# Kernel tuning notes

Measured on AMD Instinct MI355X. Metric: run time of the kernel, lower is better.

## Reference

```python
import jax, jax.numpy as jnp
import numpy as np

N_NODES = 500_000
N_EDGES = 8_000_000
BN_EPS = 1e-5


def _graph_embed(src, dst, n, W_init, b_init, Wg, bg, Wt1, g1, b1, Wt2, g2, b2, Wd, bd):
    # init_graph: input is all-ones [n, 12] -> Linear(12->4); every row identical
    x_row = W_init.sum(0) + b_init                      # [4]
    h_row = jax.nn.sigmoid(x_row @ Wg + bg)             # node gating -> [7]
    h = jnp.broadcast_to(h_row, (n, h_row.shape[0]))    # [n, 7]

    # symmetric normalization, DGL TAGConv style
    deg = jnp.zeros((n,), jnp.float32).at[dst].add(1.0)
    norm = jnp.clip(deg, 1.0) ** -0.5                   # [n]

    def prop(x):  # x: [n, d] -> normalized adjacency propagation
        x = x * norm[:, None]
        agg = jnp.zeros_like(x).at[dst].add(x[src])
        return agg * norm[:, None]

    def tagconv(x, W):  # K=2: concat [h, Ah, A^2h] then linear (no bias)
        f1 = prop(x)
        f2 = prop(f1)
        return jnp.concatenate([x, f1, f2], axis=1) @ W

    def bn_relu(x, gamma, beta):  # BatchNorm1d training-mode (batch stats)
        m = x.mean(0)
        v = x.var(0)
        return jax.nn.relu((x - m) / jnp.sqrt(v + BN_EPS) * gamma + beta)

    h = bn_relu(tagconv(h, Wt1), g1, b1)
    h = bn_relu(tagconv(h, Wt2), g2, b2)
    h = h @ Wd + bd                                     # [n, 11]
    return h.mean(0)                                    # [11] graph embedding


def setup_inputs() -> dict:
    key = jax.random.key(0)
    ks = jax.random.split(key, 32)
    n, e = N_NODES, N_EDGES
    d = {
        "src1": jax.random.randint(ks[0], (e,), 0, n, dtype=jnp.int32),
        "dst1": jax.random.randint(ks[1], (e,), 0, n, dtype=jnp.int32),
        "src2": jax.random.randint(ks[2], (e,), 0, n, dtype=jnp.int32),
        "dst2": jax.random.randint(ks[3], (e,), 0, n, dtype=jnp.int32),
        "n_nodes": n,
    }
    def w(k, shape):
        return jax.random.normal(k, shape, jnp.float32) * 0.1
    # GraphEmbed params (node_emb=4, size_graph_emb=11, layers=(7,7), TAGConv K=2)
    d["W_init"] = w(ks[4], (12, 4)); d["b_init"] = w(ks[5], (4,))
    d["Wg"] = w(ks[6], (4, 7));      d["bg"] = w(ks[7], (7,))
    d["Wt1"] = w(ks[8], (21, 7))
    d["bn1_g"] = jnp.ones((7,), jnp.float32); d["bn1_b"] = jnp.zeros((7,), jnp.float32)
    d["Wt2"] = w(ks[9], (21, 7))
    d["bn2_g"] = jnp.ones((7,), jnp.float32); d["bn2_b"] = jnp.zeros((7,), jnp.float32)
    d["Wd"] = w(ks[10], (7, 11));    d["bd"] = w(ks[11], (11,))
    # GraphSimilarity params (embedding_space=11, layers=(7,7,7), 12 properties)
    d["Ws0"] = w(ks[12], (22, 7));   d["bs0"] = w(ks[13], (7,))
    d["Ws1"] = w(ks[14], (7, 7));    d["bs1"] = w(ks[15], (7,))
    d["Ws2"] = w(ks[16], (7, 7));    d["bs2"] = w(ks[17], (7,))
    d["Ws3"] = w(ks[18], (7, 7));    d["bs3"] = w(ks[19], (7,))
    d["Wsim"] = w(ks[20], (7, 12));  d["bsim"] = w(ks[21], (12,))
    return d


def reference(src1, dst1, src2, dst2, n_nodes,
              W_init, b_init, Wg, bg, Wt1, bn1_g, bn1_b, Wt2, bn2_g, bn2_b, Wd, bd,
              Ws0, bs0, Ws1, bs1, Ws2, bs2, Ws3, bs3, Wsim, bsim):
    emb = lambda s, t: _graph_embed(s, t, n_nodes, W_init, b_init, Wg, bg,
                                    Wt1, bn1_g, bn1_b, Wt2, bn2_g, bn2_b, Wd, bd)
    hg1 = emb(src1, dst1)
    hg2 = emb(src2, dst2)
    h = jnp.concatenate([hg1, hg2])[None, :]            # [1, 22]
    h = h @ Ws0 + bs0
    for W, b in ((Ws1, bs1), (Ws2, bs2), (Ws3, bs3)):
        h = jax.nn.relu(h @ W + b)
    logits = h @ Wsim + bsim                            # [1, 12]
    # sigmoid on locality logit and sigmoid on remaining diffs == elementwise sigmoid
    return jax.nn.sigmoid(logits)
```

## Files before the change

### kernel.cpp

```cpp
#include <hip/hip_runtime.h>
#include <hip/hip_bf16.h>
#include <hip/hip_fp16.h>
#include <math.h>

#define NNODES 500000
#define BN_EPS 1e-5f
#define BKT 512
#define NBKT ((NNODES + BKT - 1) / BKT)
#define EPB 16384

__device__ __forceinline__ int atomAddI(int* p, int v) {
    return __hip_atomic_fetch_add(p, v, __ATOMIC_RELAXED, __HIP_MEMORY_SCOPE_AGENT);
}
__device__ __forceinline__ void atomAddD(double* p, double v) {
    __hip_atomic_fetch_add(p, v, __ATOMIC_RELAXED, __HIP_MEMORY_SCOPE_AGENT);
}
__device__ __forceinline__ void ldsAddF(float* p, float v) {
    __hip_atomic_fetch_add(p, v, __ATOMIC_RELAXED, __HIP_MEMORY_SCOPE_WORKGROUP);
}

template<int CNT>
__device__ __forceinline__ void blk_reduce_atomic(double (&vals)[CNT], double* dst) {
    __shared__ double sh[CNT][8];
    int lane = threadIdx.x & 63, wid = threadIdx.x >> 6;
#pragma unroll
    for (int k = 0; k < CNT; ++k) {
        double v = vals[k];
#pragma unroll
        for (int o = 32; o; o >>= 1) v += __shfl_down(v, o);
        if (lane == 0) sh[k][wid] = v;
    }
    __syncthreads();
    if ((int)threadIdx.x < CNT) {
        double v = 0.0;
#pragma unroll
        for (int w = 0; w < 8; ++w) v += sh[threadIdx.x][w];
        atomAddD(dst + threadIdx.x, v);
    }
}

__global__ void k_t0(const float* __restrict__ Wi, const float* __restrict__ bi,
                     const float* __restrict__ Wg, const float* __restrict__ bg,
                     const float* __restrict__ Wt1, float* __restrict__ fs) {
    if (threadIdx.x || blockIdx.x) return;
    float xr[4];
    for (int j = 0; j < 4; ++j) {
        float s = bi[j];
        for (int k = 0; k < 12; ++k) s += Wi[k * 4 + j];
        xr[j] = s;
    }
    float hr[7];
    for (int j = 0; j < 7; ++j) {
        float s = bg[j];
        for (int k = 0; k < 4; ++k) s += xr[k] * Wg[k * 7 + j];
        hr[j] = 1.f / (1.f + expf(-s));
        fs[j] = hr[j];
    }
    for (int j = 0; j < 7; ++j) {
        float s0 = 0.f, s1 = 0.f, s2 = 0.f;
        for (int k = 0; k < 7; ++k) {
            s0 += hr[k] * Wt1[k * 7 + j];
            s1 += hr[k] * Wt1[(7 + k) * 7 + j];
            s2 += hr[k] * Wt1[(14 + k) * 7 + j];
        }
        fs[7 + j] = s0; fs[14 + j] = s1; fs[21 + j] = s2;
    }
}

__global__ void __launch_bounds__(512) k_bhist(const int* __restrict__ dst, int* __restrict__ gcnt, int E) {
    __shared__ int h[NBKT];
    for (int i = threadIdx.x; i < NBKT; i += 512) h[i] = 0;
    __syncthreads();
    int base = blockIdx.x * EPB;
#pragma unroll
    for (int k = 0; k < EPB / 2048; ++k) {
        int i4 = base + (k * 512 + threadIdx.x) * 4;
        if (i4 + 3 < E) {
            int4 d = *reinterpret_cast<const int4*>(dst + i4);
            atomicAdd(&h[d.x >> 9], 1); atomicAdd(&h[d.y >> 9], 1);
            atomicAdd(&h[d.z >> 9], 1); atomicAdd(&h[d.w >> 9], 1);
        } else {
            for (int i = i4; i < E && i < i4 + 4; ++i) atomicAdd(&h[dst[i] >> 9], 1);
        }
    }
    __syncthreads();
    for (int i = threadIdx.x; i < NBKT; i += 512)
        if (h[i]) atomAddI(gcnt + i, h[i]);
}

__global__ void __launch_bounds__(1024) k_bscan(const int* __restrict__ gcnt,
                                                int* __restrict__ bb, int* __restrict__ gcur) {
    __shared__ int sh[1024];
    int t = threadIdx.x;
    int v = (t < NBKT) ? gcnt[t] : 0;
    sh[t] = v; __syncthreads();
    for (int o = 1; o < 1024; o <<= 1) {
        int x = (t >= o) ? sh[t - o] : 0;
        __syncthreads();
        sh[t] += x;
        __syncthreads();
    }
    if (t < NBKT) { int ex = sh[t] - v; bb[t] = ex; gcur[t] = ex; }
    if (t == 0) bb[NBKT] = sh[1023];
}

__global__ void __launch_bounds__(512) k_bscat(const int* __restrict__ src, const int* __restrict__ dst,
                                               int* __restrict__ gcur, unsigned int* __restrict__ pairs, int E) {
    __shared__ int h[NBKT];
    for (int i = threadIdx.x; i < NBKT; i += 512) h[i] = 0;
    __syncthreads();
    int base = blockIdx.x * EPB;
#pragma unroll
    for (int k = 0; k < EPB / 2048; ++k) {
        int i4 = base + (k * 512 + threadIdx.x) * 4;
        if (i4 + 3 < E) {
            int4 d = *reinterpret_cast<const int4*>(dst + i4);
            atomicAdd(&h[d.x >> 9], 1); atomicAdd(&h[d.y >> 9], 1);
            atomicAdd(&h[d.z >> 9], 1); atomicAdd(&h[d.w >> 9], 1);
        } else {
            for (int i = i4; i < E && i < i4 + 4; ++i) atomicAdd(&h[dst[i] >> 9], 1);
        }
    }
    __syncthreads();
    for (int i = threadIdx.x; i < NBKT; i += 512) {
        int c = h[i];
        h[i] = c ? atomAddI(gcur + i, c) : 0;
    }
    __syncthreads();
#pragma unroll
    for (int k = 0; k < EPB / 2048; ++k) {
        int i4 = base + (k * 512 + threadIdx.x) * 4;
        if (i4 + 3 < E) {
            int4 s = *reinterpret_cast<const int4*>(src + i4);
            int4 d = *reinterpret_cast<const int4*>(dst + i4);
            int se[4] = {s.x, s.y, s.z, s.w};
            int de[4] = {d.x, d.y, d.z, d.w};
#pragma unroll
            for (int e = 0; e < 4; ++e) {
                int b = de[e] >> 9;
                int pos = atomicAdd(&h[b], 1);
                pairs[pos] = ((unsigned int)(de[e] & 511) << 19) | (unsigned int)se[e];
            }
        } else {
            for (int i = i4; i < E && i < i4 + 4; ++i) {
                int b = dst[i] >> 9;
                int pos = atomicAdd(&h[b], 1);
                pairs[pos] = ((unsigned int)(dst[i] & 511) << 19) | (unsigned int)src[i];
            }
        }
    }
}

__global__ void __launch_bounds__(512) k_deg(const unsigned int* __restrict__ pairs, const int* __restrict__ bb,
                                             float* __restrict__ nrm, float* __restrict__ sc4, int n) {
    __shared__ int deg[BKT];
    int b = blockIdx.x, t = threadIdx.x;
    deg[t] = 0;
    __syncthreads();
    int lo = bb[b], hi = bb[b + 1];
    int k = lo + t;
    for (; k + 3 * BKT < hi; k += 4 * BKT) {
        unsigned int v1 = pairs[k], v2 = pairs[k + BKT];
        unsigned int v3 = pairs[k + 2 * BKT], v4 = pairs[k + 3 * BKT];
        atomicAdd(&deg[v1 >> 19], 1); atomicAdd(&deg[v2 >> 19], 1);
        atomicAdd(&deg[v3 >> 19], 1); atomicAdd(&deg[v4 >> 19], 1);
    }
    for (; k < hi; k += BKT) atomicAdd(&deg[pairs[k] >> 19], 1);
    __syncthreads();
    int node = b * BKT + t;
    if (node < n) {
        float sd = sqrtf((float)(deg[t] > 0 ? deg[t] : 1));
        float nn = 1.f / sd;
        nrm[node] = nn;
        reinterpret_cast<float4*>(sc4)[node] = make_float4(0.f, 0.f, nn, sd);
    }
}

__global__ void __launch_bounds__(512) k_s1(const unsigned int* __restrict__ pairs, const int* __restrict__ bb,
                                            const float* __restrict__ nrm, float* __restrict__ s1,
                                            float* __restrict__ s1n, float* __restrict__ sc4, int n) {
    __shared__ float acc[BKT];
    int b = blockIdx.x, t = threadIdx.x;
    acc[t] = 0.f;
    __syncthreads();
    int lo = bb[b], hi = bb[b + 1];
    int k = lo + t;
    for (; k + 3 * BKT < hi; k += 4 * BKT) {
        unsigned int v1 = pairs[k], v2 = pairs[k + BKT];
        unsigned int v3 = pairs[k + 2 * BKT], v4 = pairs[k + 3 * BKT];
        float g1 = nrm[v1 & 0x7FFFF], g2 = nrm[v2 & 0x7FFFF];
        float g3 = nrm[v3 & 0x7FFFF], g4 = nrm[v4 & 0x7FFFF];
        ldsAddF(&acc[v1 >> 19], g1); ldsAddF(&acc[v2 >> 19], g2);
        ldsAddF(&acc[v3 >> 19], g3); ldsAddF(&acc[v4 >> 19], g4);
    }
    for (; k < hi; k += BKT) { unsigned int v = pairs[k]; ldsAddF(&acc[v >> 19], nrm[v & 0x7FFFF]); }
    __syncthreads();
    int node = b * BKT + t;
    if (node < n) {
        float nn = nrm[node], v1 = acc[t] * nn;
        s1[node] = v1; s1n[node] = v1 * nn;
        sc4[(size_t)node * 4 + 0] = v1;
    }
}

__global__ void __launch_bounds__(512) k_s2(const unsigned int* __restrict__ pairs, const int* __restrict__ bb,
                                            const float* __restrict__ nrm, const float* __restrict__ s1,
                                            const float* __restrict__ s1n, float* __restrict__ sc4,
                                            float* __restrict__ sch, double* __restrict__ ds, int n) {
    __shared__ float acc[BKT];
    int b = blockIdx.x, t = threadIdx.x;
    acc[t] = 0.f;
    __syncthreads();
    int lo = bb[b], hi = bb[b + 1];
    int k = lo + t;
    for (; k + 3 * BKT < hi; k += 4 * BKT) {
        unsigned int v1 = pairs[k], v2 = pairs[k + BKT];
        unsigned int v3 = pairs[k + 2 * BKT], v4 = pairs[k + 3 * BKT];
        float g1 = s1n[v1 & 0x7FFFF], g2 = s1n[v2 & 0x7FFFF];
        float g3 = s1n[v3 & 0x7FFFF], g4 = s1n[v4 & 0x7FFFF];
        ldsAddF(&acc[v1 >> 19], g1); ldsAddF(&acc[v2 >> 19], g2);
        ldsAddF(&acc[v3 >> 19], g3); ldsAddF(&acc[v4 >> 19], g4);
    }
    for (; k < hi; k += BKT) { unsigned int v = pairs[k]; ldsAddF(&acc[v >> 19], s1n[v & 0x7FFFF]); }
    __syncthreads();
    double m[5] = {0, 0, 0, 0, 0};
    int node = b * BKT + t;
    if (node < n) {
        float nn = nrm[node], v2 = acc[t] * nn;
        sc4[(size_t)node * 4 + 1] = v2;
        float v1 = s1[node];
        __half2 p0 = __floats2half2_rn(v1, v2);
        __half2 p1 = __floats2half2_rn(nn, 0.f);
        float2 packed = make_float2(__uint_as_float(*(unsigned int*)&p0),
                                    __uint_as_float(*(unsigned int*)&p1));
        reinterpret_cast<float2*>(sch)[node] = packed;
        m[0] += v1; m[1] += v2;
        m[2] += (double)v1 * (double)v1;
        m[3] += (double)v2 * (double)v2;
        m[4] += (double)v1 * (double)v2;
    }
    blk_reduce_atomic<5>(m, ds);
}

__global__ void k_t1(const double* __restrict__ ds, const float* __restrict__ fs,
                     const float* __restrict__ g1, const float* __restrict__ b1, float* __restrict__ fsg) {
    if (threadIdx.x || blockIdx.x) return;
    const double inv_n = 1.0 / (double)NNODES;
    float mu1 = (float)(ds[0] * inv_n), mu2 = (float)(ds[1] * inv_n);
    float V11 = (float)(ds[2] * inv_n) - mu1 * mu1;
    float V22 = (float)(ds[3] * inv_n) - mu2 * mu2;
    float V12 = (float)(ds[4] * inv_n) - mu1 * mu2;
    for (int j = 0; j < 7; ++j) {
        float a1 = fs[14 + j], a2 = fs[21 + j];
        float var = a1 * a1 * V11 + a2 * a2 * V22 + 2.f * a1 * a2 * V12;
        float ig = (1.f / sqrtf(var + BN_EPS)) * g1[j];
        fsg[j]      = b1[j] - (mu1 * a1 + mu2 * a2) * ig;
        fsg[7 + j]  = a1 * ig;
        fsg[14 + j] = a2 * ig;
    }
}

__device__ __forceinline__ void f1_edge(const float2 r, const float* dc, float (&sarr)[7][BKT], int dl) {
    unsigned int u0 = __float_as_uint(r.x), u1 = __float_as_uint(r.y);
    __half2 h0 = *(__half2*)&u0, h1v = *(__half2*)&u1;
    float2 q0 = __half22float2(h0), q1 = __half22float2(h1v);
    float S1 = q0.x, S2 = q0.y, Nn = q1.x;
#pragma unroll
    for (int j = 0; j < 7; ++j) {
        float h = fmaxf(dc[j] + S1 * dc[7 + j] + S2 * dc[14 + j], 0.f) * Nn;
        ldsAddF(&sarr[j][dl], h);
    }
}

__global__ void __launch_bounds__(512) k_f1(const unsigned int* __restrict__ pairs, const int* __restrict__ bb,
                                            const float* __restrict__ nrm, const float* __restrict__ sch,
                                            const float* __restrict__ fsg, float* __restrict__ f1nh, int n) {
    __shared__ float a[7][BKT];
    int b = blockIdx.x, t = threadIdx.x;
    float dc[21];
#pragma unroll
    for (int j = 0; j < 21; ++j) dc[j] = fsg[j];
#pragma unroll
    for (int j = 0; j < 7; ++j) a[j][t] = 0.f;
    __syncthreads();
    int lo = bb[b], hi = bb[b + 1];
    int k = lo + t;
    for (; k + 3 * BKT < hi; k += 4 * BKT) {
        unsigned int v1 = pairs[k], v2 = pairs[k + BKT];
        unsigned int v3 = pairs[k + 2 * BKT], v4 = pairs[k + 3 * BKT];
        float2 r1 = reinterpret_cast<const float2*>(sch)[v1 & 0x7FFFF];
        float2 r2 = reinterpret_cast<const float2*>(sch)[v2 & 0x7FFFF];
        float2 r3 = reinterpret_cast<const float2*>(sch)[v3 & 0x7FFFF];
        float2 r4 = reinterpret_cast<const float2*>(sch)[v4 & 0x7FFFF];
        f1_edge(r1, dc, a, v1 >> 19);
        f1_edge(r2, dc, a, v2 >> 19);
        f1_edge(r3, dc, a, v3 >> 19);
        f1_edge(r4, dc, a, v4 >> 19);
    }
    for (; k < hi; k += BKT) {
        unsigned int v = pairs[k];
        float2 r = reinterpret_cast<const float2*>(sch)[v & 0x7FFFF];
        f1_edge(r, dc, a, v >> 19);
    }
    __syncthreads();
    int node = b * BKT + t;
    if (node < n) {
        float nn = nrm[node], sc = nn * nn;
        __half2 hh[4];
        hh[0] = __floats2half2_rn(a[0][t] * sc, a[1][t] * sc);
        hh[1] = __floats2half2_rn(a[2][t] * sc, a[3][t] * sc);
        hh[2] = __floats2half2_rn(a[4][t] * sc, a[5][t] * sc);
        hh[3] = __floats2half2_rn(a[6][t] * sc, 0.f);
        reinterpret_cast<float4*>(f1nh)[node] = *reinterpret_cast<float4*>(hh);
    }
}

__device__ __forceinline__ void x2_edge(const float4 raw, float (&sarr)[7][BKT], int dl) {
    const __half2* hp = reinterpret_cast<const __half2*>(&raw);
    float2 q0 = __half22float2(hp[0]), q1 = __half22float2(hp[1]);
    float2 q2 = __half22float2(hp[2]), q3 = __half22float2(hp[3]);
    ldsAddF(&sarr[0][dl], q0.x); ldsAddF(&sarr[1][dl], q0.y); ldsAddF(&sarr[2][dl], q1.x);
    ldsAddF(&sarr[3][dl], q1.y); ldsAddF(&sarr[4][dl], q2.x); ldsAddF(&sarr[5][dl], q2.y);
    ldsAddF(&sarr[6][dl], q3.x);
}

__global__ void __launch_bounds__(512) k_x2f(const unsigned int* __restrict__ pairs, const int* __restrict__ bb,
                                             const float* __restrict__ sc4, const float* __restrict__ fsg,
                                             const float* __restrict__ f1nh, const float* __restrict__ Wt2,
                                             float* __restrict__ x2o, double* __restrict__ ds, int n) {
    __shared__ float a[7][BKT];
    __shared__ float w[147];
    int b = blockIdx.x, t = threadIdx.x;
    for (int k = t; k < 147; k += 512) w[k] = Wt2[k];
    float dc[21];
#pragma unroll
    for (int j = 0; j < 21; ++j) dc[j] = fsg[j];
#pragma unroll
    for (int j = 0; j < 7; ++j) a[j][t] = 0.f;
    __syncthreads();
    int lo = bb[b], hi = bb[b + 1];
    int k = lo + t;
    for (; k + 3 * BKT < hi; k += 4 * BKT) {
        unsigned int v1 = pairs[k], v2 = pairs[k + BKT];
        unsigned int v3 = pairs[k + 2 * BKT], v4 = pairs[k + 3 * BKT];
        float4 r1 = reinterpret_cast<const float4*>(f1nh)[v1 & 0x7FFFF];
        float4 r2 = reinterpret_cast<const float4*>(f1nh)[v2 & 0x7FFFF];
        float4 r3 = reinterpret_cast<const float4*>(f1nh)[v3 & 0x7FFFF];
        float4 r4 = reinterpret_cast<const float4*>(f1nh)[v4 & 0x7FFFF];
        x2_edge(r1, a, v1 >> 19);
        x2_edge(r2, a, v2 >> 19);
        x2_edge(r3, a, v3 >> 19);
        x2_edge(r4, a, v4 >> 19);
    }
    for (; k < hi; k += BKT) {
        unsigned int v = pairs[k];
        float4 raw = reinterpret_cast<const float4*>(f1nh)[v & 0x7FFFF];
        x2_edge(raw, a, v >> 19);
    }
    __syncthreads();
    double sx[7] = {0, 0, 0, 0, 0, 0, 0}, sq[7] = {0, 0, 0, 0, 0, 0, 0};
    int node = b * BKT + t;
    if (node < n) {
        float4 s = reinterpret_cast<const float4*>(sc4)[node];
        float S1 = s.x, S2 = s.y, Nn = s.z, rn = s.w;
        float h1[7];
#pragma unroll
        for (int kk = 0; kk < 7; ++kk) h1[kk] = fmaxf(dc[kk] + S1 * dc[7 + kk] + S2 * dc[14 + kk], 0.f);
        float4 raw = reinterpret_cast<const float4*>(f1nh)[node];
        const __half2* hp = reinterpret_cast<const __half2*>(&raw);
        float2 q0 = __half22float2(hp[0]), q1 = __half22float2(hp[1]);
        float2 q2 = __half22float2(hp[2]), q3 = __half22float2(hp[3]);
        float f1p[7] = {q0.x * rn, q0.y * rn, q1.x * rn, q1.y * rn, q2.x * rn, q2.y * rn, q3.x * rn};
        float f2p[7];
#pragma unroll
        for (int kk = 0; kk < 7; ++kk) f2p[kk] = a[kk][t] * Nn;
        float x2[8];
#pragma unroll
        for (int j = 0; j < 7; ++j) {
            float sacc = 0.f;
#pragma unroll
            for (int kk = 0; kk < 7; ++kk)
                sacc += h1[kk] * w[kk * 7 + j] + f1p[kk] * w[(7 + kk) * 7 + j] + f2p[kk] * w[(14 + kk) * 7 + j];
            x2[j] = sacc;
            sx[j] += sacc; sq[j] += (double)sacc * (double)sacc;
        }
        x2[7] = 0.f;
        float4* q = reinterpret_cast<float4*>(x2o + (size_t)node * 8);
        q[0] = make_float4(x2[0], x2[1], x2[2], x2[3]);
        q[1] = make_float4(x2[4], x2[5], x2[6], x2[7]);
    }
    double acc[14];
#pragma unroll
    for (int j = 0; j < 7; ++j) { acc[j] = sx[j]; acc[7 + j] = sq[j]; }
    blk_reduce_atomic<14>(acc, ds + 5);
}

__global__ void k_t2(const double* __restrict__ ds, const float* __restrict__ g2,
                     const float* __restrict__ b2, float* __restrict__ fsg) {
    if (threadIdx.x || blockIdx.x) return;
    const double inv_n = 1.0 / (double)NNODES;
    for (int j = 0; j < 7; ++j) {
        float m = (float)(ds[5 + j] * inv_n);
        float v = (float)(ds[12 + j] * inv_n) - m * m;
        float ig = (1.f / sqrtf(v + BN_EPS)) * g2[j];
        fsg[21 + j] = b2[j] - m * ig;
        fsg[28 + j] = ig;
    }
}

__global__ void __launch_bounds__(512) k_h2sum(const float* __restrict__ x2o, const float* __restrict__ fsg,
                                               double* __restrict__ ds, int n) {
    float c0[7], c1[7];
#pragma unroll
    for (int j = 0; j < 7; ++j) { c0[j] = fsg[21 + j]; c1[j] = fsg[28 + j]; }
    double acc[7] = {0, 0, 0, 0, 0, 0, 0};
    for (int i = blockIdx.x * blockDim.x + threadIdx.x; i < n; i += gridDim.x * blockDim.x) {
        const float4* p = reinterpret_cast<const float4*>(x2o + (size_t)i * 8);
        float4 a = p[0], b = p[1];
        float x[7] = {a.x, a.y, a.z, a.w, b.x, b.y, b.z};
#pragma unroll
        for (int j = 0; j < 7; ++j) acc[j] += (double)fmaxf(x[j] * c1[j] + c0[j], 0.f);
    }
    blk_reduce_atomic<7>(acc, ds + 19);
}

__global__ void k_final(const double* __restrict__ ds, const float* __restrict__ Wd, const float* __restrict__ bd,
                        const float* __restrict__ Ws0, const float* __restrict__ bs0,
                        const float* __restrict__ Ws1, const float* __restrict__ bs1,
                        const float* __restrict__ Ws2, const float* __restrict__ bs2,
                        const float* __restrict__ Ws3, const float* __restrict__ bs3,
                        const float* __restrict__ Wsim, const float* __restrict__ bsim,
                        float* __restrict__ out) {
    if (threadIdx.x || blockIdx.x) return;
    const double inv_n = 1.0 / (double)NNODES;
    float v[22];
    for (int g = 0; g < 2; ++g) {
        float hm[7];
        for (int j = 0; j < 7; ++j) hm[j] = (float)(ds[g * 26 + 19 + j] * inv_n);
        for (int r = 0; r < 11; ++r) {
            float s = bd[r];
            for (int j = 0; j < 7; ++j) s += hm[j] * Wd[j * 11 + r];
            v[g * 11 + r] = s;
        }
    }
    float h[7], h2[7];
    for (int j = 0; j < 7; ++j) {
        float s = bs0[j];
        for (int k = 0; k < 22; ++k) s += v[k] * Ws0[k * 7 + j];
        h[j] = s;
    }
    const float* Ws[3] = {Ws1, Ws2, Ws3};
    const float* bs[3] = {bs1, bs2, bs3};
    for (int l = 0; l < 3; ++l) {
        for (int j = 0; j < 7; ++j) {
            float s = bs[l][j];
            for (int k = 0; k < 7; ++k) s += h[k] * Ws[l][k * 7 + j];
            h2[j] = fmaxf(s, 0.f);
        }
        for (int j = 0; j < 7; ++j) h[j] = h2[j];
    }
    for (int r = 0; r < 12; ++r) {
        float s = bsim[r];
        for (int j = 0; j < 7; ++j) s += h[j] * Wsim[j * 12 + r];
        out[r] = 1.f / (1.f + expf(-s));
    }
}

extern "C" void kernel_launch(void* const* d_in, const int* in_sizes, int n_in,
                              void* d_out, int out_size, void* d_ws, size_t ws_size,
                              hipStream_t stream) {
    const int E = in_sizes[0];
    const int n = NNODES;
    const int* src1 = (const int*)d_in[0];
    const int* dst1 = (const int*)d_in[1];
    const int* src2 = (const int*)d_in[2];
    const int* dst2 = (const int*)d_in[3];
    const float* W_init = (const float*)d_in[5];
    const float* b_init = (const float*)d_in[6];
    const float* Wg  = (const float*)d_in[7];
    const float* bg  = (const float*)d_in[8];
    const float* Wt1 = (const float*)d_in[9];
    const float* g1  = (const float*)d_in[10];
    const float* b1  = (const float*)d_in[11];
    const float* Wt2 = (const float*)d_in[12];
    const float* g2  = (const float*)d_in[13];
    const float* b2  = (const float*)d_in[14];
    const float* Wd  = (const float*)d_in[15];
    const float* bd  = (const float*)d_in[16];
    const float* Ws0 = (const float*)d_in[17];
    const float* bs0 = (const float*)d_in[18];
    const float* Ws1 = (const float*)d_in[19];
    const float* bs1 = (const float*)d_in[20];
    const float* Ws2 = (const float*)d_in[21];
    const float* bs2 = (const float*)d_in[22];
    const float* Ws3 = (const float*)d_in[23];
    const float* bs3 = (const float*)d_in[24];
    const float* Wsim = (const float*)d_in[25];
    const float* bsim = (const float*)d_in[26];

    double* dscal = (double*)d_ws;
    float* fscal  = (float*)(dscal + 52);
    float* F      = (float*)((char*)d_ws + 1024);
    float* nrm  = F;
    float* s1   = F + (size_t)n;
    float* s1n  = F + 2 * (size_t)n;
    float* sc4  = F + 3 * (size_t)n;
    float* sch  = F + 7 * (size_t)n;
    float* f1nh = F + 9 * (size_t)n;
    float* x2o  = F + 13 * (size_t)n;
    int*   gcnt = (int*)(F + 21 * (size_t)n);
    int*   bb   = gcnt + NBKT;
    int*   gcur = bb + NBKT + 1;
    unsigned int* pairs = (unsigned int*)(gcur + NBKT);

    const int EB = (E + EPB - 1) / EPB;

    hipMemsetAsync(dscal, 0, 52 * sizeof(double), stream);
    k_t0<<<1, 1, 0, stream>>>(W_init, b_init, Wg, bg, Wt1, fscal);

    for (int g = 0; g < 2; ++g) {
        const int* src = g ? src2 : src1;
        const int* dst = g ? dst2 : dst1;
        float* fsg  = fscal + 28 + g * 35;
        double* dsg = dscal + g * 26;

        hipMemsetAsync(gcnt, 0, NBKT * sizeof(int), stream);
        k_bhist<<<EB, 512, 0, stream>>>(dst, gcnt, E);
        k_bscan<<<1, 1024, 0, stream>>>(gcnt, bb, gcur);
        k_bscat<<<EB, 512, 0, stream>>>(src, dst, gcur, pairs, E);

        k_deg<<<NBKT, 512, 0, stream>>>(pairs, bb, nrm, sc4, n);
        k_s1 <<<NBKT, 512, 0, stream>>>(pairs, bb, nrm, s1, s1n, sc4, n);
        k_s2 <<<NBKT, 512, 0, stream>>>(pairs, bb, nrm, s1, s1n, sc4, sch, dsg, n);
        k_t1<<<1, 1, 0, stream>>>(dsg, fscal, g1, b1, fsg);
        k_f1 <<<NBKT, 512, 0, stream>>>(pairs, bb, nrm, sch, fsg, f1nh, n);
        k_x2f<<<NBKT, 512, 0, stream>>>(pairs, bb, sc4, fsg, f1nh, Wt2, x2o, dsg, n);
        k_t2<<<1, 1, 0, stream>>>(dsg, g2, b2, fsg);
        k_h2sum<<<512, 512, 0, stream>>>(x2o, fsg, dsg, n);
    }
    k_final<<<1, 1, 0, stream>>>(dscal, Wd, bd, Ws0, bs0, Ws1, bs1, Ws2, bs2, Ws3, bs3,
                                 Wsim, bsim, (float*)d_out);
}
```

Measured before the change: 2.011 ms.

## Quantize propagated features to 8-bit floats and halve destination bucket size

Replaces the fp16 packed per-node f1 feature (16 bytes) with a custom 8-bit log-like encoding packed into 8 bytes, halving the gather traffic in the second propagation pass. It also shrinks destination buckets from 512 to 256 nodes, doubling the number of buckets and blocks, and adapts the scan kernel to handle two buckets per thread. The 8-bit code keeps only 4 mantissa bits and a limited exponent range, so accuracy drops and small values flush to zero.

```diff
diff --git a/kernel.cpp b/kernel.cpp
--- a/kernel.cpp
+++ b/kernel.cpp
@@ -5,7 +5,7 @@
 
 #define NNODES 500000
 #define BN_EPS 1e-5f
-#define BKT 512
+#define BKT 256
 #define NBKT ((NNODES + BKT - 1) / BKT)
 #define EPB 16384
 
@@ -19,9 +19,23 @@
     __hip_atomic_fetch_add(p, v, __ATOMIC_RELAXED, __HIP_MEMORY_SCOPE_WORKGROUP);
 }
 
-template<int CNT>
+__device__ __forceinline__ unsigned enc8(float x) {
+    unsigned u = __float_as_uint(x);
+    u += (1u << 18);
+    int e = (int)(u >> 23) - 127;
+    if (e < -8) return 0u;
+    unsigned code = ((unsigned)(e + 8) << 4) | ((u >> 19) & 0xFu);
+    return code > 255u ? 255u : code;
+}
+__device__ __forceinline__ float dec8(unsigned c) {
+    if (c == 0u) return 0.f;
+    unsigned bits = (((c >> 4) + 119u) << 23) | ((c & 0xFu) << 19);
+    return __uint_as_float(bits);
+}
+
+template<int CNT, int W>
 __device__ __forceinline__ void blk_reduce_atomic(double (&vals)[CNT], double* dst) {
-    __shared__ double sh[CNT][8];
+    __shared__ double sh[CNT][W];
     int lane = threadIdx.x & 63, wid = threadIdx.x >> 6;
 #pragma unroll
     for (int k = 0; k < CNT; ++k) {
@@ -34,7 +48,7 @@
     if ((int)threadIdx.x < CNT) {
         double v = 0.0;
 #pragma unroll
-        for (int w = 0; w < 8; ++w) v += sh[threadIdx.x][w];
+        for (int w = 0; w < W; ++w) v += sh[threadIdx.x][w];
         atomAddD(dst + threadIdx.x, v);
     }
 }
@@ -77,10 +91,10 @@
         int i4 = base + (k * 512 + threadIdx.x) * 4;
         if (i4 + 3 < E) {
             int4 d = *reinterpret_cast<const int4*>(dst + i4);
-            atomicAdd(&h[d.x >> 9], 1); atomicAdd(&h[d.y >> 9], 1);
-            atomicAdd(&h[d.z >> 9], 1); atomicAdd(&h[d.w >> 9], 1);
+            atomicAdd(&h[d.x >> 8], 1); atomicAdd(&h[d.y >> 8], 1);
+            atomicAdd(&h[d.z >> 8], 1); atomicAdd(&h[d.w >> 8], 1);
         } else {
-            for (int i = i4; i < E && i < i4 + 4; ++i) atomicAdd(&h[dst[i] >> 9], 1);
+            for (int i = i4; i < E && i < i4 + 4; ++i) atomicAdd(&h[dst[i] >> 8], 1);
         }
     }
     __syncthreads();
@@ -92,16 +106,21 @@
                                                 int* __restrict__ bb, int* __restrict__ gcur) {
     __shared__ int sh[1024];
     int t = threadIdx.x;
-    int v = (t < NBKT) ? gcnt[t] : 0;
-    sh[t] = v; __syncthreads();
+    int i0 = 2 * t, i1 = 2 * t + 1;
+    int c0 = (i0 < NBKT) ? gcnt[i0] : 0;
+    int c1 = (i1 < NBKT) ? gcnt[i1] : 0;
+    int s = c0 + c1;
+    sh[t] = s; __syncthreads();
     for (int o = 1; o < 1024; o <<= 1) {
         int x = (t >= o) ? sh[t - o] : 0;
         __syncthreads();
         sh[t] += x;
         __syncthreads();
     }
-    if (t < NBKT) { int ex = sh[t] - v; bb[t] = ex; gcur[t] = ex; }
-    if (t == 0) bb[NBKT] = sh[1023];
+    int ex = sh[t] - s;
+    if (i0 < NBKT) { bb[i0] = ex; gcur[i0] = ex; }
+    if (i1 < NBKT) { bb[i1] = ex + c0; gcur[i1] = ex + c0; }
+    if (t == 1023) bb[NBKT] = sh[1023];
 }
 
 __global__ void __launch_bounds__(512) k_bscat(const int* __restrict__ src, const int* __restrict__ dst,
@@ -115,10 +134,10 @@
         int i4 = base + (k * 512 + threadIdx.x) * 4;
         if (i4 + 3 < E) {
             int4 d = *reinterpret_cast<const int4*>(dst + i4);
-            atomicAdd(&h[d.x >> 9], 1); atomicAdd(&h[d.y >> 9], 1);
-            atomicAdd(&h[d.z >> 9], 1); atomicAdd(&h[d.w >> 9], 1);
+            atomicAdd(&h[d.x >> 8], 1); atomicAdd(&h[d.y >> 8], 1);
+            atomicAdd(&h[d.z >> 8], 1); atomicAdd(&h[d.w >> 8], 1);
         } else {
-            for (int i = i4; i < E && i < i4 + 4; ++i) atomicAdd(&h[dst[i] >> 9], 1);
+            for (int i = i4; i < E && i < i4 + 4; ++i) atomicAdd(&h[dst[i] >> 8], 1);
         }
     }
     __syncthreads();
@@ -137,21 +156,21 @@
             int de[4] = {d.x, d.y, d.z, d.w};
 #pragma unroll
             for (int e = 0; e < 4; ++e) {
-                int b = de[e] >> 9;
+                int b = de[e] >> 8;
                 int pos = atomicAdd(&h[b], 1);
-                pairs[pos] = ((unsigned int)(de[e] & 511) << 19) | (unsigned int)se[e];
+                pairs[pos] = ((unsigned int)(de[e] & 255) << 19) | (unsigned int)se[e];
             }
         } else {
             for (int i = i4; i < E && i < i4 + 4; ++i) {
-                int b = dst[i] >> 9;
+                int b = dst[i] >> 8;
                 int pos = atomicAdd(&h[b], 1);
-                pairs[pos] = ((unsigned int)(dst[i] & 511) << 19) | (unsigned int)src[i];
+                pairs[pos] = ((unsigned int)(dst[i] & 255) << 19) | (unsigned int)src[i];
             }
         }
     }
 }
 
-__global__ void __launch_bounds__(512) k_deg(const unsigned int* __restrict__ pairs, const int* __restrict__ bb,
+__global__ void __launch_bounds__(256) k_deg(const unsigned int* __restrict__ pairs, const int* __restrict__ bb,
                                              float* __restrict__ nrm, float* __restrict__ sc4, int n) {
     __shared__ int deg[BKT];
     int b = blockIdx.x, t = threadIdx.x;
@@ -176,7 +195,7 @@
     }
 }
 
-__global__ void __launch_bounds__(512) k_s1(const unsigned int* __restrict__ pairs, const int* __restrict__ bb,
+__global__ void __launch_bounds__(256) k_s1(const unsigned int* __restrict__ pairs, const int* __restrict__ bb,
                                             const float* __restrict__ nrm, float* __restrict__ s1,
                                             float* __restrict__ s1n, float* __restrict__ sc4, int n) {
     __shared__ float acc[BKT];
@@ -203,7 +222,7 @@
     }
 }
 
-__global__ void __launch_bounds__(512) k_s2(const unsigned int* __restrict__ pairs, const int* __restrict__ bb,
+__global__ void __launch_bounds__(256) k_s2(const unsigned int* __restrict__ pairs, const int* __restrict__ bb,
                                             const float* __restrict__ nrm, const float* __restrict__ s1,
                                             const float* __restrict__ s1n, float* __restrict__ sc4,
                                             float* __restrict__ sch, double* __restrict__ ds, int n) {
@@ -239,7 +258,7 @@
         m[3] += (double)v2 * (double)v2;
         m[4] += (double)v1 * (double)v2;
     }
-    blk_reduce_atomic<5>(m, ds);
+    blk_reduce_atomic<5, 4>(m, ds);
 }
 
 __global__ void k_t1(const double* __restrict__ ds, const float* __restrict__ fs,
@@ -272,9 +291,9 @@
     }
 }
 
-__global__ void __launch_bounds__(512) k_f1(const unsigned int* __restrict__ pairs, const int* __restrict__ bb,
+__global__ void __launch_bounds__(256) k_f1(const unsigned int* __restrict__ pairs, const int* __restrict__ bb,
                                             const float* __restrict__ nrm, const float* __restrict__ sch,
-                                            const float* __restrict__ fsg, float* __restrict__ f1nh, int n) {
+                                            const float* __restrict__ fsg, unsigned int* __restrict__ f1q, int n) {
     __shared__ float a[7][BKT];
     int b = blockIdx.x, t = threadIdx.x;
     float dc[21];
@@ -306,32 +325,35 @@
     int node = b * BKT + t;
     if (node < n) {
         float nn = nrm[node], sc = nn * nn;
-        __half2 hh[4];
-        hh[0] = __floats2half2_rn(a[0][t] * sc, a[1][t] * sc);
-        hh[1] = __floats2half2_rn(a[2][t] * sc, a[3][t] * sc);
-        hh[2] = __floats2half2_rn(a[4][t] * sc, a[5][t] * sc);
-        hh[3] = __floats2half2_rn(a[6][t] * sc, 0.f);
-        reinterpret_cast<float4*>(f1nh)[node] = *reinterpret_cast<float4*>(hh);
-    }
-}
-
-__device__ __forceinline__ void x2_edge(const float4 raw, float (&sarr)[7][BKT], int dl) {
-    const __half2* hp = reinterpret_cast<const __half2*>(&raw);
-    float2 q0 = __half22float2(hp[0]), q1 = __half22float2(hp[1]);
-    float2 q2 = __half22float2(hp[2]), q3 = __half22float2(hp[3]);
-    ldsAddF(&sarr[0][dl], q0.x); ldsAddF(&sarr[1][dl], q0.y); ldsAddF(&sarr[2][dl], q1.x);
-    ldsAddF(&sarr[3][dl], q1.y); ldsAddF(&sarr[4][dl], q2.x); ldsAddF(&sarr[5][dl], q2.y);
-    ldsAddF(&sarr[6][dl], q3.x);
-}
-
-__global__ void __launch_bounds__(512) k_x2f(const unsigned int* __restrict__ pairs, const int* __restrict__ bb,
+        unsigned c0 = enc8(a[0][t] * sc), c1 = enc8(a[1][t] * sc);
+        unsigned c2 = enc8(a[2][t] * sc), c3 = enc8(a[3][t] * sc);
+        unsigned c4 = enc8(a[4][t] * sc), c5 = enc8(a[5][t] * sc);
+        unsigned c6 = enc8(a[6][t] * sc);
+        uint2 packed;
+        packed.x = c0 | (c1 << 8) | (c2 << 16) | (c3 << 24);
+        packed.y = c4 | (c5 << 8) | (c6 << 16);
+        reinterpret_cast<uint2*>(f1q)[node] = packed;
+    }
+}
+
+__device__ __forceinline__ void x2_edge(const uint2 r, float (&sarr)[7][BKT], int dl) {
+    ldsAddF(&sarr[0][dl], dec8(r.x & 255u));
+    ldsAddF(&sarr[1][dl], dec8((r.x >> 8) & 255u));
+    ldsAddF(&sarr[2][dl], dec8((r.x >> 16) & 255u));
+    ldsAddF(&sarr[3][dl], dec8(r.x >> 24));
+    ldsAddF(&sarr[4][dl], dec8(r.y & 255u));
+    ldsAddF(&sarr[5][dl], dec8((r.y >> 8) & 255u));
+    ldsAddF(&sarr[6][dl], dec8((r.y >> 16) & 255u));
+}
+
+__global__ void __launch_bounds__(256) k_x2f(const unsigned int* __restrict__ pairs, const int* __restrict__ bb,
                                              const float* __restrict__ sc4, const float* __restrict__ fsg,
-                                             const float* __restrict__ f1nh, const float* __restrict__ Wt2,
+                                             const unsigned int* __restrict__ f1q, const float* __restrict__ Wt2,
                                              float* __restrict__ x2o, double* __restrict__ ds, int n) {
     __shared__ float a[7][BKT];
     __shared__ float w[147];
     int b = blockIdx.x, t = threadIdx.x;
-    for (int k = t; k < 147; k += 512) w[k] = Wt2[k];
+    for (int k = t; k < 147; k += 256) w[k] = Wt2[k];
     float dc[21];
 #pragma unroll
     for (int j = 0; j < 21; ++j) dc[j] = fsg[j];
@@ -343,10 +365,10 @@
     for (; k + 3 * BKT < hi; k += 4 * BKT) {
         unsigned int v1 = pairs[k], v2 = pairs[k + BKT];
         unsigned int v3 = pairs[k + 2 * BKT], v4 = pairs[k + 3 * BKT];
-        float4 r1 = reinterpret_cast<const float4*>(f1nh)[v1 & 0x7FFFF];
-        float4 r2 = reinterpret_cast<const float4*>(f1nh)[v2 & 0x7FFFF];
-        float4 r3 = reinterpret_cast<const float4*>(f1nh)[v3 & 0x7FFFF];
-        float4 r4 = reinterpret_cast<const float4*>(f1nh)[v4 & 0x7FFFF];
+        uint2 r1 = reinterpret_cast<const uint2*>(f1q)[v1 & 0x7FFFF];
+        uint2 r2 = reinterpret_cast<const uint2*>(f1q)[v2 & 0x7FFFF];
+        uint2 r3 = reinterpret_cast<const uint2*>(f1q)[v3 & 0x7FFFF];
+        uint2 r4 = reinterpret_cast<const uint2*>(f1q)[v4 & 0x7FFFF];
         x2_edge(r1, a, v1 >> 19);
         x2_edge(r2, a, v2 >> 19);
         x2_edge(r3, a, v3 >> 19);
@@ -354,7 +376,7 @@
     }
     for (; k < hi; k += BKT) {
         unsigned int v = pairs[k];
-        float4 raw = reinterpret_cast<const float4*>(f1nh)[v & 0x7FFFF];
+        uint2 raw = reinterpret_cast<const uint2*>(f1q)[v & 0x7FFFF];
         x2_edge(raw, a, v >> 19);
     }
     __syncthreads();
@@ -366,11 +388,11 @@
         float h1[7];
 #pragma unroll
         for (int kk = 0; kk < 7; ++kk) h1[kk] = fmaxf(dc[kk] + S1 * dc[7 + kk] + S2 * dc[14 + kk], 0.f);
-        float4 raw = reinterpret_cast<const float4*>(f1nh)[node];
-        const __half2* hp = reinterpret_cast<const __half2*>(&raw);
-        float2 q0 = __half22float2(hp[0]), q1 = __half22float2(hp[1]);
-        float2 q2 = __half22float2(hp[2]), q3 = __half22float2(hp[3]);
-        float f1p[7] = {q0.x * rn, q0.y * rn, q1.x * rn, q1.y * rn, q2.x * rn, q2.y * rn, q3.x * rn};
+        uint2 raw = reinterpret_cast<const uint2*>(f1q)[node];
+        float f1p[7] = {dec8(raw.x & 255u) * rn, dec8((raw.x >> 8) & 255u) * rn,
+                        dec8((raw.x >> 16) & 255u) * rn, dec8(raw.x >> 24) * rn,
+                        dec8(raw.y & 255u) * rn, dec8((raw.y >> 8) & 255u) * rn,
+                        dec8((raw.y >> 16) & 255u) * rn};
         float f2p[7];
 #pragma unroll
         for (int kk = 0; kk < 7; ++kk) f2p[kk] = a[kk][t] * Nn;
@@ -392,7 +414,7 @@
     double acc[14];
 #pragma unroll
     for (int j = 0; j < 7; ++j) { acc[j] = sx[j]; acc[7 + j] = sq[j]; }
-    blk_reduce_atomic<14>(acc, ds + 5);
+    blk_reduce_atomic<14, 4>(acc, ds + 5);
 }
 
 __global__ void k_t2(const double* __restrict__ ds, const float* __restrict__ g2,
@@ -421,7 +443,7 @@
 #pragma unroll
         for (int j = 0; j < 7; ++j) acc[j] += (double)fmaxf(x[j] * c1[j] + c0[j], 0.f);
     }
-    blk_reduce_atomic<7>(acc, ds + 19);
+    blk_reduce_atomic<7, 8>(acc, ds + 19);
 }
 
 __global__ void k_final(const double* __restrict__ ds, const float* __restrict__ Wd, const float* __restrict__ bd,
@@ -506,9 +528,9 @@
     float* s1n  = F + 2 * (size_t)n;
     float* sc4  = F + 3 * (size_t)n;
     float* sch  = F + 7 * (size_t)n;
-    float* f1nh = F + 9 * (size_t)n;
-    float* x2o  = F + 13 * (size_t)n;
-    int*   gcnt = (int*)(F + 21 * (size_t)n);
+    unsigned int* f1q = (unsigned int*)(F + 9 * (size_t)n);
+    float* x2o  = F + 11 * (size_t)n;
+    int*   gcnt = (int*)(F + 19 * (size_t)n);
     int*   bb   = gcnt + NBKT;
     int*   gcur = bb + NBKT + 1;
     unsigned int* pairs = (unsigned int*)(gcur + NBKT);
@@ -529,12 +551,12 @@
         k_bscan<<<1, 1024, 0, stream>>>(gcnt, bb, gcur);
         k_bscat<<<EB, 512, 0, stream>>>(src, dst, gcur, pairs, E);
 
-        k_deg<<<NBKT, 512, 0, stream>>>(pairs, bb, nrm, sc4, n);
-        k_s1 <<<NBKT, 512, 0, stream>>>(pairs, bb, nrm, s1, s1n, sc4, n);
-        k_s2 <<<NBKT, 512, 0, stream>>>(pairs, bb, nrm, s1, s1n, sc4, sch, dsg, n);
+        k_deg<<<NBKT, 256, 0, stream>>>(pairs, bb, nrm, sc4, n);
+        k_s1 <<<NBKT, 256, 0, stream>>>(pairs, bb, nrm, s1, s1n, sc4, n);
+        k_s2 <<<NBKT, 256, 0, stream>>>(pairs, bb, nrm, s1, s1n, sc4, sch, dsg, n);
         k_t1<<<1, 1, 0, stream>>>(dsg, fscal, g1, b1, fsg);
-        k_f1 <<<NBKT, 512, 0, stream>>>(pairs, bb, nrm, sch, fsg, f1nh, n);
-        k_x2f<<<NBKT, 512, 0, stream>>>(pairs, bb, sc4, fsg, f1nh, Wt2, x2o, dsg, n);
+        k_f1 <<<NBKT, 256, 0, stream>>>(pairs, bb, nrm, sch, fsg, f1q, n);
+        k_x2f<<<NBKT, 256, 0, stream>>>(pairs, bb, sc4, fsg, f1q, Wt2, x2o, dsg, n);
         k_t2<<<1, 1, 0, stream>>>(dsg, g2, b2, fsg);
         k_h2sum<<<512, 512, 0, stream>>>(x2o, fsg, dsg, n);
     }
```

After: 2.045 ms. No clear change (+1.7%).
